# Kernel optimization log

Hardware: AMD Instinct MI355X
Metric: run time of the kernel (lower is better)

## Reference

```python
import jax, jax.numpy as jnp
import numpy as np

# Wong-Wang-Deco neural mass parameters (whobpyt defaults)
G=20.0; LAMBDA=0.0; A_E=310.0; B_E=125.0; D_E=0.16; TAU_E=100.0; W_E=1.0
A_I=615.0; B_I=177.0; D_I=0.087; TAU_I=10.0; W_I=0.7
W_PLUS=1.4; J_NMDA=0.15; J=1.0; GAMMA=0.641e-3; GAMMA_I=1.0e-3
SIG=0.01; I_0=0.382; I_EXT=0.0
DT=0.0001  # step_size
N_REGIONS=512; N_STEPS=20000


def _H(I, a, b, d, big_c):
    # firing-rate transfer function H_for_*_V3
    x = a * I - b
    numer = jnp.abs(x) + 1e-9
    neg = -d * x
    denom = jnp.where(
        neg > 50.0,
        jnp.abs(1.0 - big_c * neg) + 1e-9 * d,
        jnp.abs(1.0 - jnp.exp(jnp.minimum(neg, 51.0))) + 1e-9 * d,
    )
    return numer / denom


def setup_inputs() -> dict:
    key = jax.random.key(0)
    k1, k2, k3 = jax.random.split(key, 3)
    init_state = jax.random.uniform(k1, (N_REGIONS, 2), dtype=jnp.float32) * 0.2
    # row-normalized random structural connectivity
    Con_Mtx = jax.random.uniform(k2, (N_REGIONS, N_REGIONS), dtype=jnp.float32) / N_REGIONS
    v_of_T = jax.random.normal(k3, (N_STEPS, N_REGIONS), dtype=jnp.float32)
    return {"init_state": init_state, "Con_Mtx": Con_Mtx, "v_of_T": v_of_T}


def reference(init_state, Con_Mtx, v_of_T):
    S_E0 = init_state[:, 0]
    S_I0 = init_state[:, 1]

    def step(carry, v):
        S_E, S_I = carry
        Network_S_E = Con_Mtx @ S_E  # [N]
        I_E = W_E * I_0 + W_PLUS * J_NMDA * S_E + G * J_NMDA * Network_S_E - J * S_I + I_EXT
        I_I = W_I * I_0 + J_NMDA * S_E - S_I + LAMBDA * G * J_NMDA * Network_S_E
        r_E = _H(I_E, A_E, B_E, D_E, 1e9)
        r_I = _H(I_I, A_I, B_I, D_I, 1e5)
        dS_E = -S_E / TAU_E + (1.0 - S_E) * GAMMA * r_E + SIG * v
        dS_I = -S_I / TAU_I + GAMMA_I * r_I + SIG * v
        S_E = S_E + DT * dS_E
        S_I = S_I + DT * dS_I
        return (S_E, S_I), jnp.stack([S_E, S_I], axis=1)  # [N,2]

    (S_E, S_I), state_hist = jax.lax.scan(step, (S_E0, S_I0), v_of_T)
    state_vals = jnp.stack([S_E, S_I], axis=1)  # [N,2]
    return state_vals, state_hist  # ([N,2], [T,N,2])
```

## Files before the change

kernel.cpp:

```cpp
#include <hip/hip_runtime.h>
#include <cstdint>

#define NREG 512
#define NBLK 8
#define NTHR 512

typedef unsigned long long u64;
typedef unsigned int u32;

__device__ __forceinline__ float Hfun(float I, float a, float b, float d, float bigc) {
    float x = a * I - b;
    float numer = fabsf(x) + 1e-9f;
    float neg = -d * x;
    float denom;
    if (neg > 50.0f) {
        denom = fabsf(1.0f - bigc * neg) + 1e-9f * d;
    } else {
        denom = fabsf(1.0f - expf(fminf(neg, 51.0f))) + 1e-9f * d;
    }
    return numer / denom;
}

__global__ __launch_bounds__(NTHR, 1)
void rww_kernel(const float* __restrict__ init_state,
                const float* __restrict__ Con,
                const float* __restrict__ v_of_T,
                float* __restrict__ out,
                u64* __restrict__ xslot,
                int nsteps)
{
    __shared__ __align__(16) float buf[2][NREG];

    const int tid = threadIdx.x;
    const int w   = tid >> 6;
    const int l   = tid & 63;
    const int s   = l & 7;
    const int rl  = l >> 3;
    const int b   = blockIdx.x;
    const int row = b * 64 + w * 8 + rl;
    const int rot = s << 1;

    float2* __restrict__ state2 = reinterpret_cast<float2*>(out);
    float2* __restrict__ hist2  = reinterpret_cast<float2*>(out + 2 * NREG);

    float4 cw[16];
#pragma unroll
    for (int k = 0; k < 16; ++k) {
        int c = s * 64 + (((k + rot) & 15) << 2);
        cw[k] = *reinterpret_cast<const float4*>(Con + (size_t)row * NREG + c);
    }
#pragma unroll
    for (int k = 0; k < 16; ++k)
        asm volatile("" : "+v"(cw[k].x), "+v"(cw[k].y), "+v"(cw[k].z), "+v"(cw[k].w));

    buf[0][tid] = init_state[2 * tid];
    float sEo  = init_state[2 * row];
    float sIo  = init_state[2 * row + 1];
    float vcur = v_of_T[row];
    __syncthreads();

    for (int t = 0; t < nsteps; ++t) {
        float vnext = 0.f;
        if (t + 1 < nsteps) vnext = v_of_T[(size_t)(t + 1) * NREG + row];

        const int p = t & 1;
        const float* sb = &buf[p][s << 6];
        float a0 = 0.f, a1 = 0.f, a2 = 0.f, a3 = 0.f;
#pragma unroll
        for (int j = 0; j < 16; ++j) {
            float4 sv = *reinterpret_cast<const float4*>(sb + (((j + rot) & 15) << 2));
            a0 = fmaf(cw[j].x, sv.x, a0);
            a1 = fmaf(cw[j].y, sv.y, a1);
            a2 = fmaf(cw[j].z, sv.z, a2);
            a3 = fmaf(cw[j].w, sv.w, a3);
        }
        float net = (a0 + a1) + (a2 + a3);
        net += __shfl_xor(net, 1, 64);
        net += __shfl_xor(net, 2, 64);
        net += __shfl_xor(net, 4, 64);

        float I_E = 0.382f + 0.21f * sEo + 3.0f * net - sIo;
        float rE  = Hfun(I_E, 310.0f, 125.0f, 0.16f, 1.0e9f);
        float dSE = -sEo * 0.01f + (1.0f - sEo) * 0.000641f * rE + 0.01f * vcur;
        float sEn = sEo + 1e-4f * dSE;

        const int pn = (t + 1) & 1;
        u64 pk = ((u64)(u32)(t + 1) << 32) | (u64)__float_as_uint(sEn);
        if (s == 0) {
            __hip_atomic_store(&xslot[pn * NREG + row], pk,
                               __ATOMIC_RELAXED, __HIP_MEMORY_SCOPE_AGENT);
            buf[pn][row] = sEn;
        }

        float I_I = 0.2674f + 0.15f * sEo - sIo;
        float rI  = Hfun(I_I, 615.0f, 177.0f, 0.087f, 1.0e5f);
        float dSI = -sIo * 0.1f + 0.001f * rI + 0.01f * vcur;
        float sIn = sIo + 1e-4f * dSI;
        if (s == 0) {
            hist2[(size_t)t * NREG + row] = make_float2(sEn, sIn);
            if (t == nsteps - 1) state2[row] = make_float2(sEn, sIn);
        }
        sEo = sEn; sIo = sIn; vcur = vnext;

        if (t + 1 < nsteps && (tid >> 6) != b) {
            u64* slot = &xslot[pn * NREG + tid];
            const u32 want = (u32)(t + 1);
            u64 pk2;
            int spins = 0;
            for (;;) {
                pk2 = __hip_atomic_load(slot, __ATOMIC_RELAXED, __HIP_MEMORY_SCOPE_AGENT);
                if ((u32)(pk2 >> 32) == want) break;
                if (++spins > 256) {
                    __builtin_amdgcn_s_sleep(2);
                    spins = 0;
                }
            }
            buf[pn][tid] = __uint_as_float((u32)pk2);
        }

        asm volatile("s_waitcnt lgkmcnt(0)" ::: "memory");
        __builtin_amdgcn_s_barrier();
    }
}

extern "C" void kernel_launch(void* const* d_in, const int* in_sizes, int n_in,
                              void* d_out, int out_size, void* d_ws, size_t ws_size,
                              hipStream_t stream) {
    const float* init_state = (const float*)d_in[0];
    const float* Con        = (const float*)d_in[1];
    const float* v_of_T     = (const float*)d_in[2];
    int nsteps = in_sizes[2] / NREG;

    rww_kernel<<<dim3(NBLK), dim3(NTHR), 0, stream>>>(
        init_state, Con, v_of_T, (float*)d_out, (u64*)d_ws, nsteps);
}
```

Baseline: 33.20 ms.

## Elect eight workgroups on one XCC and exchange state via L2-local flags

Launches 256 workgroups. The first eight that land on the same XCC (read from the hardware XCC id register) are elected as workers and the rest exit, so the per-step cross-block exchange can stay within one XCC's L2. Each step it publishes a 32-bit value with a 4-bit step tag in the low mantissa bits, stored and loaded with sc0 global ops, and falls back to the agent-scope 64-bit slot after a bounded number of tries. The Con rows are no longer held in registers; they are reloaded from global memory every step. Risks: the tag truncates the low 4 mantissa bits of the exchanged S_E, there is an extra memset and launch cost, and the per-step Con reloads add memory traffic.

```diff
diff --git a/kernel.cpp b/kernel.cpp
--- a/kernel.cpp
+++ b/kernel.cpp
@@ -1,9 +1,12 @@
 #include <hip/hip_runtime.h>
 #include <cstdint>
 
-#define NREG 512
-#define NBLK 8
-#define NTHR 512
+#define NREG    512
+#define NTHR    512
+#define NWORK   8
+#define NLAUNCH 256
+#define FAST_TRIES 1024
+#define ELECT_TRIES (1 << 20)
 
 typedef unsigned long long u64;
 typedef unsigned int u32;
@@ -13,12 +16,21 @@
     float numer = fabsf(x) + 1e-9f;
     float neg = -d * x;
     float denom;
-    if (neg > 50.0f) {
-        denom = fabsf(1.0f - bigc * neg) + 1e-9f * d;
-    } else {
-        denom = fabsf(1.0f - expf(fminf(neg, 51.0f))) + 1e-9f * d;
-    }
+    if (neg > 50.0f) denom = fabsf(1.0f - bigc * neg) + 1e-9f * d;
+    else             denom = fabsf(1.0f - expf(fminf(neg, 51.0f))) + 1e-9f * d;
     return numer / denom;
+}
+
+__device__ __forceinline__ u32 load_u32_sc0(const u32* p) {
+    u32 v;
+    asm volatile("global_load_dword %0, %1, off sc0\n\t"
+                 "s_waitcnt vmcnt(0)"
+                 : "=v"(v) : "v"(p) : "memory");
+    return v;
+}
+__device__ __forceinline__ void store_u32_sc0(u32* p, u32 v) {
+    asm volatile("global_store_dword %0, %1, off sc0"
+                 :: "v"(p), "v"(v) : "memory");
 }
 
 __global__ __launch_bounds__(NTHR, 1)
@@ -26,32 +38,54 @@
                 const float* __restrict__ Con,
                 const float* __restrict__ v_of_T,
                 float* __restrict__ out,
-                u64* __restrict__ xslot,
+                void* __restrict__ wsv,
                 int nsteps)
 {
+    char* wsb   = (char*)wsv;
+    u32* cnt    = (u32*)wsb;
+    u32* winner = (u32*)(wsb + 32);
+    u64* slow   = (u64*)(wsb + 64);
+    u32* fast   = (u32*)(wsb + 8256);
+
+    __shared__ u32 sel;
     __shared__ __align__(16) float buf[2][NREG];
 
     const int tid = threadIdx.x;
+
+    if (tid == 0) {
+        u32 xcc;
+        asm volatile("s_getreg_b32 %0, hwreg(HW_REG_XCC_ID, 0, 32)" : "=s"(xcc));
+        xcc &= 7u;
+        u32 tick = atomicAdd(&cnt[xcc], 1u);
+        if (tick == NWORK - 1) atomicCAS(winner, 0u, xcc + 1u);
+        u32 wv = 0; int tries = 0;
+        for (;;) {
+            wv = __hip_atomic_load(winner, __ATOMIC_RELAXED, __HIP_MEMORY_SCOPE_AGENT);
+            if (wv != 0u) break;
+            if (++tries > ELECT_TRIES) break;
+            if ((tries & 63) == 0) __builtin_amdgcn_s_sleep(2);
+        }
+        u32 r;
+        if (wv != 0u) r = (xcc == wv - 1u && tick < NWORK) ? tick : 0xFFu;
+        else          r = (blockIdx.x < NWORK) ? (blockIdx.x | 0x100u) : 0xFFu;
+        sel = r;
+    }
+    __syncthreads();
+    const u32 selv = sel;
+    if ((selv & 0xFFu) == 0xFFu) return;
+    const u32 wid = selv & 0xFFu;
+    bool useSlow = (selv & 0x100u) != 0u;
+
     const int w   = tid >> 6;
     const int l   = tid & 63;
     const int s   = l & 7;
     const int rl  = l >> 3;
-    const int b   = blockIdx.x;
-    const int row = b * 64 + w * 8 + rl;
+    const int row = (int)wid * 64 + w * 8 + rl;
     const int rot = s << 1;
 
-    float2* __restrict__ state2 = reinterpret_cast<float2*>(out);
-    float2* __restrict__ hist2  = reinterpret_cast<float2*>(out + 2 * NREG);
-
-    float4 cw[16];
-#pragma unroll
-    for (int k = 0; k < 16; ++k) {
-        int c = s * 64 + (((k + rot) & 15) << 2);
-        cw[k] = *reinterpret_cast<const float4*>(Con + (size_t)row * NREG + c);
-    }
-#pragma unroll
-    for (int k = 0; k < 16; ++k)
-        asm volatile("" : "+v"(cw[k].x), "+v"(cw[k].y), "+v"(cw[k].z), "+v"(cw[k].w));
+    float2* state2 = reinterpret_cast<float2*>(out);
+    float2* hist2  = reinterpret_cast<float2*>(out + 2 * NREG);
+    const float4* conrow = reinterpret_cast<const float4*>(Con + (size_t)row * NREG);
 
     buf[0][tid] = init_state[2 * tid];
     float sEo  = init_state[2 * row];
@@ -68,11 +102,13 @@
         float a0 = 0.f, a1 = 0.f, a2 = 0.f, a3 = 0.f;
 #pragma unroll
         for (int j = 0; j < 16; ++j) {
-            float4 sv = *reinterpret_cast<const float4*>(sb + (((j + rot) & 15) << 2));
-            a0 = fmaf(cw[j].x, sv.x, a0);
-            a1 = fmaf(cw[j].y, sv.y, a1);
-            a2 = fmaf(cw[j].z, sv.z, a2);
-            a3 = fmaf(cw[j].w, sv.w, a3);
+            int jj = (j + rot) & 15;
+            float4 cv = conrow[(s << 4) + jj];
+            float4 sv = *reinterpret_cast<const float4*>(sb + (jj << 2));
+            a0 = fmaf(cv.x, sv.x, a0);
+            a1 = fmaf(cv.y, sv.y, a1);
+            a2 = fmaf(cv.z, sv.z, a2);
+            a3 = fmaf(cv.w, sv.w, a3);
         }
         float net = (a0 + a1) + (a2 + a3);
         net += __shfl_xor(net, 1, 64);
@@ -85,9 +121,11 @@
         float sEn = sEo + 1e-4f * dSE;
 
         const int pn = (t + 1) & 1;
-        u64 pk = ((u64)(u32)(t + 1) << 32) | (u64)__float_as_uint(sEn);
         if (s == 0) {
-            __hip_atomic_store(&xslot[pn * NREG + row], pk,
+            u32 fb = (__float_as_uint(sEn) & ~0xFu) | ((u32)(t + 1) & 0xFu);
+            store_u32_sc0(&fast[pn * NREG + row], fb);
+            u64 pk = ((u64)(u32)(t + 1) << 32) | (u64)__float_as_uint(sEn);
+            __hip_atomic_store(&slow[pn * NREG + row], pk,
                                __ATOMIC_RELAXED, __HIP_MEMORY_SCOPE_AGENT);
             buf[pn][row] = sEn;
         }
@@ -102,24 +140,35 @@
         }
         sEo = sEn; sIo = sIn; vcur = vnext;
 
-        if (t + 1 < nsteps && (tid >> 6) != b) {
-            u64* slot = &xslot[pn * NREG + tid];
-            const u32 want = (u32)(t + 1);
-            u64 pk2;
-            int spins = 0;
-            for (;;) {
-                pk2 = __hip_atomic_load(slot, __ATOMIC_RELAXED, __HIP_MEMORY_SCOPE_AGENT);
-                if ((u32)(pk2 >> 32) == want) break;
-                if (++spins > 256) {
-                    __builtin_amdgcn_s_sleep(2);
-                    spins = 0;
+        if (t + 1 < nsteps && (u32)w != wid) {
+            float val = 0.f; bool got = false;
+            if (!useSlow) {
+                const u32 want4 = (u32)(t + 1) & 0xFu;
+                int tries = 0;
+                for (;;) {
+                    u32 bits = load_u32_sc0(&fast[pn * NREG + tid]);
+                    if ((bits & 0xFu) == want4) { val = __uint_as_float(bits); got = true; break; }
+                    if (++tries > FAST_TRIES) { useSlow = true; break; }
                 }
             }
-            buf[pn][tid] = __uint_as_float((u32)pk2);
+            if (!got) {
+                const u32 want = (u32)(t + 1);
+                u64 pk2;
+                int spins = 0;
+                for (;;) {
+                    pk2 = __hip_atomic_load(&slow[pn * NREG + tid],
+                                            __ATOMIC_RELAXED, __HIP_MEMORY_SCOPE_AGENT);
+                    if ((u32)(pk2 >> 32) == want) break;
+                    if (++spins > 256) { __builtin_amdgcn_s_sleep(2); spins = 0; }
+                }
+                val = __uint_as_float((u32)pk2);
+            }
+            buf[pn][tid] = val;
         }
 
         asm volatile("s_waitcnt lgkmcnt(0)" ::: "memory");
         __builtin_amdgcn_s_barrier();
+        asm volatile("" ::: "memory");
     }
 }
 
@@ -131,6 +180,7 @@
     const float* v_of_T     = (const float*)d_in[2];
     int nsteps = in_sizes[2] / NREG;
 
-    rww_kernel<<<dim3(NBLK), dim3(NTHR), 0, stream>>>(
-        init_state, Con, v_of_T, (float*)d_out, (u64*)d_ws, nsteps);
+    hipMemsetAsync(d_ws, 0, 16384, stream);
+    rww_kernel<<<dim3(NLAUNCH), dim3(NTHR), 0, stream>>>(
+        init_state, Con, v_of_T, (float*)d_out, d_ws, nsteps);
 }
```

After: 28.97 ms. 1.15x faster.
